# Kernel optimization log

Measured on AMD Instinct MI355X. Metric: run time of the kernel, lower is better.

The kernel has to match this reference:

```python
import jax, jax.numpy as jnp
import numpy as np


def setup_inputs() -> dict:
    key = jax.random.key(0)
    k1, k2 = jax.random.split(key)
    B, H, S, D = 2, 16, 2048, 64
    scores = jax.random.normal(k1, (B, H, S, S), dtype=jnp.float32)
    v = jax.random.normal(k2, (B, H, S, D), dtype=jnp.float32)
    return {"scores": scores, "v": v}


def reference(scores, v):
    # softmax over last dim of [B,H,S,S], then contract with V [B,H,S,D]
    prob = jax.nn.softmax(scores, axis=-1)
    return jnp.einsum('bhqk,bhkd->bhqd', prob, v)
```

## Files before the change

### kernel.cpp

```cpp
#include <hip/hip_runtime.h>
#include <hip/hip_bf16.h>

#define NBH  32
#define SEQ  2048
#define DIM  64
#define PSTR 2056

typedef __attribute__((ext_vector_type(4))) float f32x4;
typedef __attribute__((ext_vector_type(8))) short bf16x8;

__device__ __forceinline__ unsigned short bfbits(float f) {
    unsigned u = __builtin_bit_cast(unsigned, f);
    u += 0x7FFFu + ((u >> 16) & 1u);
    return (unsigned short)(u >> 16);
}
__device__ __forceinline__ unsigned pk(float a, float b) {
    return (unsigned)bfbits(a) | ((unsigned)bfbits(b) << 16);
}

__global__ __launch_bounds__(256)
void vprep_kernel(const float* __restrict__ v, unsigned short* __restrict__ wsv)
{
    const int blk = blockIdx.x;
    const int bh  = blk >> 5, tau = blk & 31;
    const float* vp = v + ((size_t)bh * SEQ + tau * 64) * DIM;
    unsigned short* op = wsv + (size_t)blk * 4096;

    for (int fl = threadIdx.x; fl < 512; fl += 256) {
        const int ks = fl >> 8, dt = (fl >> 6) & 3, lane = fl & 63;
        const int g = lane >> 4, c = lane & 15;
        const float* sp = vp + (ks * 32 + g * 8) * DIM + dt * 16 + c;
        bf16x8 frag;
#pragma unroll
        for (int j = 0; j < 8; ++j)
            frag[j] = (short)bfbits(sp[j * DIM]);
        *reinterpret_cast<bf16x8*>(op + fl * 8) = frag;
    }
}

__global__ __launch_bounds__(512, 2)
void softmaxv_kernel(const float* __restrict__ scores,
                     const unsigned short* __restrict__ vfrags,
                     float* __restrict__ out)
{
    __shared__ unsigned short P[16 * PSTR];
    __shared__ float red[4][64][8];

    const int tid  = threadIdx.x;
    const int w    = tid >> 6;
    const int lane = tid & 63;
    const int dt   = w & 3;
    const int ksub = w >> 2;
    const int g    = lane >> 4;
    const int c    = lane & 15;

    const int bid = blockIdx.x;
    const int bh  = bid & 31;
    const int s   = bid >> 5;

    const float* sblk = scores + ((size_t)bh * SEQ + s * 256) * SEQ;
    const unsigned short* vb = vfrags + (size_t)bh * 32 * 4096 + lane * 8;
    float* const oblk = out + ((size_t)bh * SEQ + s * 256) * DIM;

    bf16x8 ones;
#pragma unroll
    for (int j = 0; j < 8; ++j) ones[j] = (short)0x3F80;

    bf16x8 vreg[32];
#pragma unroll
    for (int kk = 0; kk < 32; ++kk)
        vreg[kk] = *reinterpret_cast<const bf16x8*>(
            vb + (size_t)(ksub * 32 + kk) * 2048 + dt * 512);

    const int r0 = 2 * w;
    f32x4 st[2][8];

#define ISSUE(t)                                                               \
    {                                                                          \
        _Pragma("unroll")                                                      \
        for (int rr = 0; rr < 2; ++rr)                                         \
            _Pragma("unroll")                                                  \
            for (int j = 0; j < 8; ++j)                                        \
                st[rr][j] = *reinterpret_cast<const f32x4*>(                   \
                    sblk + (size_t)((t) * 16 + r0 + rr) * SEQ +                \
                    j * 256 + (lane << 2));                                    \
    }

#define LDS_BAR asm volatile("s_waitcnt lgkmcnt(0)\n\ts_barrier" ::: "memory");

    ISSUE(0)

    for (int t = 0; t < 16; ++t) {
#pragma unroll
        for (int rr = 0; rr < 2; ++rr) {
            const int row = r0 + rr;
#pragma unroll
            for (int j = 0; j < 8; ++j) {
                const f32x4 sv = st[rr][j];
                const float e0 = __expf(sv[0]), e1 = __expf(sv[1]);
                const float e2 = __expf(sv[2]), e3 = __expf(sv[3]);
                uint2 pw = make_uint2(pk(e0, e1), pk(e2, e3));
                *reinterpret_cast<uint2*>(&P[row * PSTR + j * 256 + lane * 4]) = pw;
            }
        }
        if (t < 15) ISSUE(t + 1)

        LDS_BAR

        f32x4 acc  = (f32x4)0.0f;
        f32x4 accl = (f32x4)0.0f;
#pragma unroll
        for (int kk = 0; kk < 32; ++kk) {
            const int K = ksub * 32 + kk;
            const bf16x8 a = *reinterpret_cast<const bf16x8*>(
                &P[c * PSTR + K * 32 + g * 8]);
            acc  = __builtin_amdgcn_mfma_f32_16x16x32_bf16(a, vreg[kk], acc,  0, 0, 0);
            accl = __builtin_amdgcn_mfma_f32_16x16x32_bf16(a, ones,     accl, 0, 0, 0);
        }

        if (ksub == 1) {
            *reinterpret_cast<f32x4*>(&red[dt][lane][0]) = acc;
            *reinterpret_cast<f32x4*>(&red[dt][lane][4]) = accl;
        }

        LDS_BAR

        if (ksub == 0) {
            const f32x4 a2 = *reinterpret_cast<const f32x4*>(&red[dt][lane][0]);
            const f32x4 l2 = *reinterpret_cast<const f32x4*>(&red[dt][lane][4]);
            const f32x4 at = acc + a2;
            const f32x4 lt = accl + l2;
            float* op = oblk + (size_t)(t * 16) * DIM + dt * 16 + c;
#pragma unroll
            for (int r = 0; r < 4; ++r)
                op[(size_t)(g * 4 + r) * DIM] = at[r] * (1.0f / lt[r]);
        }
    }
#undef ISSUE
#undef LDS_BAR
}

extern "C" void kernel_launch(void* const* d_in, const int* in_sizes, int n_in,
                              void* d_out, int out_size, void* d_ws, size_t ws_size,
                              hipStream_t stream)
{
    const float* scores = (const float*)d_in[0];
    const float* v      = (const float*)d_in[1];
    float* out          = (float*)d_out;
    unsigned short* wsv = (unsigned short*)d_ws;

    vprep_kernel<<<dim3(NBH * 32), dim3(256), 0, stream>>>(v, wsv);
    softmaxv_kernel<<<dim3(256), dim3(512), 0, stream>>>(scores, wsv, out);
}
```

Before: 114.6 us.

## Stream score rows block-wide with an eight-row rolling prefetch ring

After: 115.7 us. No clear change (+1.0%).

```diff
diff --git a/kernel.cpp b/kernel.cpp
--- a/kernel.cpp
+++ b/kernel.cpp
@@ -72,38 +72,28 @@
         vreg[kk] = *reinterpret_cast<const bf16x8*>(
             vb + (size_t)(ksub * 32 + kk) * 2048 + dt * 512);
 
-    const int r0 = 2 * w;
-    f32x4 st[2][8];
+    f32x4 st[8];
 
-#define ISSUE(t)                                                               \
-    {                                                                          \
-        _Pragma("unroll")                                                      \
-        for (int rr = 0; rr < 2; ++rr)                                         \
-            _Pragma("unroll")                                                  \
-            for (int j = 0; j < 8; ++j)                                        \
-                st[rr][j] = *reinterpret_cast<const f32x4*>(                   \
-                    sblk + (size_t)((t) * 16 + r0 + rr) * SEQ +                \
-                    j * 256 + (lane << 2));                                    \
-    }
+#define LOADR(R, slot)                                                         \
+    st[slot] = *reinterpret_cast<const f32x4*>(                                \
+        sblk + (size_t)(R) * SEQ + tid * 4);
 
 #define LDS_BAR asm volatile("s_waitcnt lgkmcnt(0)\n\ts_barrier" ::: "memory");
 
-    ISSUE(0)
+    LOADR(0, 0) LOADR(1, 1) LOADR(2, 2) LOADR(3, 3)
+    LOADR(4, 4) LOADR(5, 5) LOADR(6, 6) LOADR(7, 7)
 
     for (int t = 0; t < 16; ++t) {
 #pragma unroll
-        for (int rr = 0; rr < 2; ++rr) {
-            const int row = r0 + rr;
-#pragma unroll
-            for (int j = 0; j < 8; ++j) {
-                const f32x4 sv = st[rr][j];
-                const float e0 = __expf(sv[0]), e1 = __expf(sv[1]);
-                const float e2 = __expf(sv[2]), e3 = __expf(sv[3]);
-                uint2 pw = make_uint2(pk(e0, e1), pk(e2, e3));
-                *reinterpret_cast<uint2*>(&P[row * PSTR + j * 256 + lane * 4]) = pw;
-            }
+        for (int r = 0; r < 16; ++r) {
+            const f32x4 sv = st[r & 7];
+            const int R = t * 16 + r;
+            if (R + 8 < 256) { LOADR(R + 8, r & 7) }
+            const float e0 = __expf(sv[0]), e1 = __expf(sv[1]);
+            const float e2 = __expf(sv[2]), e3 = __expf(sv[3]);
+            *reinterpret_cast<uint2*>(&P[r * PSTR + tid * 4]) =
+                make_uint2(pk(e0, e1), pk(e2, e3));
         }
-        if (t < 15) ISSUE(t + 1)
 
         LDS_BAR
 
@@ -136,7 +126,7 @@
                 op[(size_t)(g * 4 + r) * DIM] = at[r] * (1.0f / lt[r]);
         }
     }
-#undef ISSUE
+#undef LOADR
 #undef LDS_BAR
 }
 
```
